# Kernel tuning notes

Hardware: AMD Instinct MI355X
Metric: run time of the kernel (lower is better)

## Reference

```python
import jax, jax.numpy as jnp
import numpy as np

B, S, H = 1, 2048, 2048
HD, NQ, NKV = 128, 16, 4
FFH = 8192
EPS = 1e-5
ROPE_BASE = 10000.0
SOFTMAX_CAP = 50.0
CLIP_L, CLIP_R = 0.0, 1.0


def setup_inputs() -> dict:
    key = jax.random.key(0)
    ks = jax.random.split(key, 10)
    std = 0.02
    return {
        "x": jax.random.normal(ks[0], (B, S, H), dtype=jnp.float32),
        "attn_norm_w": jax.random.uniform(ks[1], (H,), minval=-1.0, maxval=1.0, dtype=jnp.float32),
        "mlp_norm_w": jax.random.uniform(ks[2], (H,), minval=-1.0, maxval=1.0, dtype=jnp.float32),
        "wq": jax.random.normal(ks[3], (H, NQ * HD), dtype=jnp.float32) * std,
        "wk": jax.random.normal(ks[4], (H, NKV * HD), dtype=jnp.float32) * std,
        "wv": jax.random.normal(ks[5], (H, NKV * HD), dtype=jnp.float32) * std,
        "wo": jax.random.normal(ks[6], (NQ * HD, H), dtype=jnp.float32) * std,
        "w_gate": jax.random.normal(ks[7], (H, FFH), dtype=jnp.float32) * std,
        "w_up": jax.random.normal(ks[8], (H, FFH), dtype=jnp.float32) * std,
        "w_down": jax.random.normal(ks[9], (FFH, H), dtype=jnp.float32) * std,
    }


def _rms_norm(x, w):
    # GroupRMSNorm with group_size=None -> whole hidden dim
    var = jnp.mean(jnp.square(x), axis=-1, keepdims=True)
    return x * jax.lax.rsqrt(var + EPS) * w


def _rope_cos_sin(seq_len, dim):
    inv_freq = 1.0 / (ROPE_BASE ** (jnp.arange(0, dim, 2, dtype=jnp.float32) / dim))
    t = jnp.arange(seq_len, dtype=jnp.float32)
    freqs = jnp.outer(t, inv_freq)                      # [S, dim/2]
    emb = jnp.concatenate([freqs, freqs], axis=-1)      # [S, dim]
    return jnp.cos(emb), jnp.sin(emb)


def _apply_rope(x, cos, sin):
    # x: [B, S, h, d]; rotate-half (LLaMA-style)
    d = x.shape[-1]
    x1, x2 = x[..., : d // 2], x[..., d // 2 :]
    rot = jnp.concatenate([-x2, x1], axis=-1)
    return x * cos[None, :, None, :] + rot * sin[None, :, None, :]


def _qk_norm(x):
    # per-head RMS norm over head_dim (qk_norm_group_size == head_dim), unit weight
    var = jnp.mean(jnp.square(x), axis=-1, keepdims=True)
    return x * jax.lax.rsqrt(var + EPS)


def reference(x, attn_norm_w, mlp_norm_w, wq, wk, wv, wo, w_gate, w_up, w_down):
    # ---- attention sub-layer ----
    h = _rms_norm(x, attn_norm_w)                                     # [B,S,H]
    q = (h @ wq).reshape(B, S, NQ, HD)
    k = (h @ wk).reshape(B, S, NKV, HD)
    v = (h @ wv).reshape(B, S, NKV, HD)

    cos, sin = _rope_cos_sin(S, HD)
    q = _apply_rope(q, cos, sin)
    k = _apply_rope(k, cos, sin)

    q = _qk_norm(q)
    k = _qk_norm(k)

    # GQA: expand kv heads to match q heads
    rep = NQ // NKV
    k = jnp.repeat(k, rep, axis=2)                                    # [B,S,NQ,HD]
    v = jnp.repeat(v, rep, axis=2)

    scale = 1.0 / jnp.sqrt(jnp.float32(HD))
    scores = jnp.einsum("bshd,bthd->bhst", q, k) * scale              # [B,NQ,S,S]
    # softmax cap: cap * tanh(s / cap)
    scores = SOFTMAX_CAP * jnp.tanh(scores / SOFTMAX_CAP)
    causal = jnp.tril(jnp.ones((S, S), dtype=bool))
    scores = jnp.where(causal[None, None], scores, -jnp.inf)
    p = jax.nn.softmax(scores, axis=-1)
    # clip range (l, r): clamp(p * (r - l) + l, 0, 1)
    p = jnp.clip(p * (CLIP_R - CLIP_L) + CLIP_L, 0.0, 1.0)
    o = jnp.einsum("bhst,bthd->bshd", p, v).reshape(B, S, NQ * HD)
    x = x + o @ wo

    # ---- MLP sub-layer (gated SiLU) ----
    h2 = _rms_norm(x, mlp_norm_w)
    mlp_out = (jax.nn.silu(h2 @ w_gate) * (h2 @ w_up)) @ w_down
    return x + mlp_out
```

## Files before the change

### kernel.cpp

```cpp
#include <hip/hip_runtime.h>

typedef __bf16 bf16;
typedef __bf16 bf16x4 __attribute__((ext_vector_type(4)));
typedef __bf16 bf16x8 __attribute__((ext_vector_type(8)));
typedef float f32x4 __attribute__((ext_vector_type(4)));

#define GLP16(gp, lp) __builtin_amdgcn_global_load_lds( \
    (const __attribute__((address_space(1))) void*)(gp), \
    (__attribute__((address_space(3))) void*)(lp), 16, 0, 0)

__device__ __forceinline__ f32x4 mfma16(bf16x8 a, bf16x8 b, f32x4 c) {
    return __builtin_amdgcn_mfma_f32_16x16x32_bf16(a, b, c, 0, 0, 0);
}

__global__ __launch_bounds__(256) void k_rmsnorm(const float* __restrict__ x,
        const float* __restrict__ w, bf16* __restrict__ out) {
    const int H = 2048;
    size_t row = blockIdx.x;
    const float* xr = x + row * H;
    int base = threadIdx.x * 8;
    float4 a = *(const float4*)(xr + base);
    float4 b = *(const float4*)(xr + base + 4);
    float ss = a.x*a.x + a.y*a.y + a.z*a.z + a.w*a.w
             + b.x*b.x + b.y*b.y + b.z*b.z + b.w*b.w;
#pragma unroll
    for (int m = 32; m > 0; m >>= 1) ss += __shfl_xor(ss, m);
    __shared__ float red[4];
    if ((threadIdx.x & 63) == 0) red[threadIdx.x >> 6] = ss;
    __syncthreads();
    float tot = red[0] + red[1] + red[2] + red[3];
    float rs = rsqrtf(tot * (1.0f / H) + 1e-5f);
    float4 wa = *(const float4*)(w + base);
    float4 wb = *(const float4*)(w + base + 4);
    bf16x8 ov;
    ov[0] = (bf16)(a.x * rs * wa.x); ov[1] = (bf16)(a.y * rs * wa.y);
    ov[2] = (bf16)(a.z * rs * wa.z); ov[3] = (bf16)(a.w * rs * wa.w);
    ov[4] = (bf16)(b.x * rs * wb.x); ov[5] = (bf16)(b.y * rs * wb.y);
    ov[6] = (bf16)(b.z * rs * wb.z); ov[7] = (bf16)(b.w * rs * wb.w);
    *(bf16x8*)(out + row * H + base) = ov;
}

__global__ __launch_bounds__(256) void k_convT(const float* __restrict__ W,
        bf16* __restrict__ Wt, int K, int N, int rmul, int roff) {
    __shared__ float t[64][65];
    int k0 = blockIdx.x * 64, n0 = blockIdx.y * 64;
    int tid = threadIdx.x;
#pragma unroll
    for (int it = 0; it < 4; it++) {
        int idx = it * 256 + tid;
        int r = idx >> 4, c = (idx & 15) * 4;
        float4 v = *(const float4*)(W + (size_t)(k0 + r) * N + n0 + c);
        t[r][c] = v.x; t[r][c + 1] = v.y; t[r][c + 2] = v.z; t[r][c + 3] = v.w;
    }
    __syncthreads();
#pragma unroll
    for (int it = 0; it < 4; it++) {
        int idx = it * 256 + tid;
        int n = idx >> 4, kc = (idx & 15) * 4;
        bf16x4 o;
#pragma unroll
        for (int j = 0; j < 4; j++) o[j] = (bf16)t[kc + j][n];
        *(bf16x4*)(Wt + ((size_t)(n0 + n) * rmul + roff) * K + k0 + kc) = o;
    }
}

__global__ __launch_bounds__(256) void k_transpose(const bf16* __restrict__ in,
        bf16* __restrict__ out, int R, int C) {
    __shared__ bf16 t[32][33];
    int r0 = blockIdx.x * 32, c0 = blockIdx.y * 32;
    int tx = threadIdx.x & 31, ty = threadIdx.x >> 5;
#pragma unroll
    for (int i = 0; i < 4; i++)
        t[ty + i * 8][tx] = in[(size_t)(r0 + ty + i * 8) * C + c0 + tx];
    __syncthreads();
#pragma unroll
    for (int i = 0; i < 4; i++)
        out[(size_t)(c0 + ty + i * 8) * R + r0 + tx] = t[tx][ty + i * 8];
}

template<int EPI>
__global__ __launch_bounds__(512, 2) void k_gemm5(const bf16* __restrict__ A,
        const bf16* __restrict__ Bt, void* __restrict__ outp,
        const void* __restrict__ aux, int M, int N, int K, int ksplit) {
    extern __shared__ char lds[];
    const int tid = threadIdx.x, wave = tid >> 6, lane = tid & 63;
    const int lr = lane & 15, kg = lane >> 4;
    const int wm = wave >> 2, wn = wave & 3;
    const int bn = blockIdx.x, bm = blockIdx.y, split = blockIdx.z;
    const int row0 = bm * 256, col0 = bn * 256;
    const int kbeg = split * ksplit;
    const int NT = ksplit >> 6;
    const size_t K2 = (size_t)K * 2;
    const int xorm = (lr & 7) << 4;

    char* const A0p = lds;
    char* const A1p = lds + 32768;
    char* const B0p = lds + 65536;
    char* const B1p = lds + 98304;

    size_t soff[2];
#pragma unroll
    for (int s = 0; s < 2; s++) {
        int d = s * 8192 + tid * 16;
        int rh = d >> 7, c = d & 127;
        soff[s] = (size_t)rh * K2 + (c ^ ((rh & 7) << 4));
    }
    const char* Ab = (const char*)A + ((size_t)row0 * K + kbeg) * 2;
    const char* Bb = (const char*)Bt + ((size_t)col0 * K + kbeg) * 2;

    auto stA = [&](int t, int mh) {
        const char* src = Ab + (size_t)(mh * 128) * K2 + (size_t)t * 128;
        char* dst = lds + (t & 1) * 32768 + mh * 16384 + wave * 1024;
        GLP16(src + soff[0], dst);
        GLP16(src + soff[1], dst + 8192);
    };
    auto stB = [&](int t, int nh) {
        const char* src = Bb + (size_t)(nh * 128) * K2 + (size_t)t * 128;
        char* dst = lds + 65536 + (t & 1) * 32768 + nh * 16384 + wave * 1024;
        GLP16(src + soff[0], dst);
        GLP16(src + soff[1], dst + 8192);
    };

    f32x4 acc[8][4];
#pragma unroll
    for (int m = 0; m < 8; m++)
#pragma unroll
        for (int n = 0; n < 4; n++) acc[m][n] = (f32x4){0, 0, 0, 0};

    bf16x8 a[8], c0[4], c1[4];
    auto rdA = [&](const char* base, int mh) {
#pragma unroll
        for (int mi = 0; mi < 4; mi++)
#pragma unroll
            for (int kk = 0; kk < 2; kk++) {
                int rh = wm * 64 + mi * 16 + lr;
                int c = (kk * 64 + kg * 16) ^ xorm;
                a[mi * 2 + kk] = *(const bf16x8*)(base + mh * 16384 + rh * 128 + c);
            }
    };
    auto rdB = [&](const char* base, int nh, bf16x8 (&b)[4]) {
#pragma unroll
        for (int nj = 0; nj < 2; nj++)
#pragma unroll
            for (int kk = 0; kk < 2; kk++) {
                int rh = wn * 32 + nj * 16 + lr;
                int c = (kk * 64 + kg * 16) ^ xorm;
                b[nj * 2 + kk] = *(const bf16x8*)(base + nh * 16384 + rh * 128 + c);
            }
    };
    auto mm = [&](int mh, int nh, bf16x8 (&b)[4]) {
#pragma unroll
        for (int mi = 0; mi < 4; mi++)
#pragma unroll
            for (int nj = 0; nj < 2; nj++)
#pragma unroll
                for (int kk = 0; kk < 2; kk++)
                    acc[mh * 4 + mi][nh * 2 + nj] =
                        mfma16(a[mi * 2 + kk], b[nj * 2 + kk],
                               acc[mh * 4 + mi][nh * 2 + nj]);
    };

#define PBAR do { asm volatile("" ::: "memory"); \
                  __builtin_amdgcn_s_barrier(); \
                  asm volatile("" ::: "memory"); } while (0)

    stA(0, 0); stB(0, 0); stB(0, 1); stA(0, 1);
    stA(1, 0); stB(1, 0); stB(1, 1);
    asm volatile("s_waitcnt vmcnt(6)" ::: "memory");
    PBAR;

    const int NIT = NT >> 1;
    for (int it = 0; it < NIT; ++it) {
        const int t = it * 2;
        const bool more = (t + 2 < NT);
        rdA(A0p, 0); rdB(B0p, 0, c0);
        stA(t + 1, 1);
        __builtin_amdgcn_s_setprio(1); mm(0, 0, c0); __builtin_amdgcn_s_setprio(0);
        PBAR;
        rdB(B0p, 1, c1);
        if (more) stA(t + 2, 0);
        __builtin_amdgcn_s_setprio(1); mm(0, 1, c1); __builtin_amdgcn_s_setprio(0);
        PBAR;
        rdA(A0p, 1);
        if (more) stB(t + 2, 0);
        __builtin_amdgcn_s_setprio(1); mm(1, 1, c1); __builtin_amdgcn_s_setprio(0);
        PBAR;
        if (more) stB(t + 2, 1);
        __builtin_amdgcn_s_setprio(1); mm(1, 0, c0); __builtin_amdgcn_s_setprio(0);
        if (more) asm volatile("s_waitcnt vmcnt(6)" ::: "memory");
        else      asm volatile("s_waitcnt vmcnt(0)" ::: "memory");
        PBAR;
        rdA(A1p, 0); rdB(B1p, 0, c0);
        if (more) stA(t + 2, 1);
        __builtin_amdgcn_s_setprio(1); mm(0, 0, c0); __builtin_amdgcn_s_setprio(0);
        PBAR;
        rdB(B1p, 1, c1);
        if (t + 3 < NT) stA(t + 3, 0);
        __builtin_amdgcn_s_setprio(1); mm(0, 1, c1); __builtin_amdgcn_s_setprio(0);
        PBAR;
        rdA(A1p, 1);
        if (t + 3 < NT) stB(t + 3, 0);
        __builtin_amdgcn_s_setprio(1); mm(1, 1, c1); __builtin_amdgcn_s_setprio(0);
        PBAR;
        if (t + 3 < NT) stB(t + 3, 1);
        __builtin_amdgcn_s_setprio(1); mm(1, 0, c0); __builtin_amdgcn_s_setprio(0);
        if (more) asm volatile("s_waitcnt vmcnt(6)" ::: "memory");
        PBAR;
    }
#undef PBAR

#pragma unroll
    for (int mi = 0; mi < 8; mi++)
#pragma unroll
        for (int ni = 0; ni < 4; ni++)
#pragma unroll
            for (int r = 0; r < 4; r++) {
                size_t row = row0 + (mi >> 2) * 128 + wm * 64 + (mi & 3) * 16 + kg * 4 + r;
                size_t col = col0 + (ni >> 1) * 128 + wn * 32 + (ni & 1) * 16 + lr;
                float vv = acc[mi][ni][r];
                if (EPI == 5) {
                    ((bf16*)outp)[(size_t)split * M * N + row * N + col] = (bf16)vv;
                } else {
                    float pv = __shfl_xor(vv, 1);
                    float g = (lane & 1) ? pv : vv;
                    float u = (lane & 1) ? vv : pv;
                    float sg = g / (1.0f + __expf(-g));
                    if (!(lane & 1))
                        ((bf16*)outp)[row * (size_t)(N >> 1) + (col >> 1)] =
                            (bf16)(sg * u);
                }
            }
}

__global__ __launch_bounds__(256) void k_reduce(const bf16* __restrict__ parts,
        const float* __restrict__ resid, float* __restrict__ out,
        int ns, size_t n8) {
    size_t i = (size_t)blockIdx.x * 256 + threadIdx.x;
    if (i >= n8) return;
    size_t base = i * 8;
    float4 a = *(const float4*)(resid + base);
    float4 b = *(const float4*)(resid + base + 4);
    for (int s = 0; s < ns; s++) {
        bf16x8 p = *(const bf16x8*)(parts + (size_t)s * n8 * 8 + base);
        a.x += (float)p[0]; a.y += (float)p[1]; a.z += (float)p[2]; a.w += (float)p[3];
        b.x += (float)p[4]; b.y += (float)p[5]; b.z += (float)p[6]; b.w += (float)p[7];
    }
    *(float4*)(out + base) = a;
    *(float4*)(out + base + 4) = b;
}

__global__ __launch_bounds__(256) void k_reduce_rms(const bf16* __restrict__ parts,
        const float* __restrict__ resid, const float* __restrict__ w,
        float* __restrict__ x2, bf16* __restrict__ hb, int ns) {
    const int H = 2048;
    size_t row = blockIdx.x;
    int base = threadIdx.x * 8;
    const float* rr = resid + row * H + base;
    float4 a = *(const float4*)rr;
    float4 b = *(const float4*)(rr + 4);
    for (int s = 0; s < ns; s++) {
        bf16x8 p = *(const bf16x8*)(parts + (size_t)s * H * 2048 + row * H + base);
        a.x += (float)p[0]; a.y += (float)p[1]; a.z += (float)p[2]; a.w += (float)p[3];
        b.x += (float)p[4]; b.y += (float)p[5]; b.z += (float)p[6]; b.w += (float)p[7];
    }
    *(float4*)(x2 + row * H + base) = a;
    *(float4*)(x2 + row * H + base + 4) = b;
    float ss = a.x*a.x + a.y*a.y + a.z*a.z + a.w*a.w
             + b.x*b.x + b.y*b.y + b.z*b.z + b.w*b.w;
#pragma unroll
    for (int m = 32; m > 0; m >>= 1) ss += __shfl_xor(ss, m);
    __shared__ float red[4];
    if ((threadIdx.x & 63) == 0) red[threadIdx.x >> 6] = ss;
    __syncthreads();
    float tot = red[0] + red[1] + red[2] + red[3];
    float rs = rsqrtf(tot * (1.0f / H) + 1e-5f);
    float4 wa = *(const float4*)(w + base);
    float4 wb = *(const float4*)(w + base + 4);
    bf16x8 ov;
    ov[0] = (bf16)(a.x * rs * wa.x); ov[1] = (bf16)(a.y * rs * wa.y);
    ov[2] = (bf16)(a.z * rs * wa.z); ov[3] = (bf16)(a.w * rs * wa.w);
    ov[4] = (bf16)(b.x * rs * wb.x); ov[5] = (bf16)(b.y * rs * wb.y);
    ov[6] = (bf16)(b.z * rs * wb.z); ov[7] = (bf16)(b.w * rs * wb.w);
    *(bf16x8*)(hb + row * H + base) = ov;
}

__global__ __launch_bounds__(256) void k_qkvrope(const bf16* __restrict__ parts,
        bf16* __restrict__ qb, bf16* __restrict__ kb, bf16* __restrict__ vb) {
    int s = blockIdx.x;
    int tid = threadIdx.x, wave = tid >> 6, lane = tid & 63;
    const bf16* p0 = parts + (size_t)s * 3072;
    const bf16* p1 = p0 + (size_t)2048 * 3072;
    float f = exp2f((float)lane * -0.2076205059304601f);
    float sn, cs;
    sincosf((float)s * f, &sn, &cs);
#pragma unroll 1
    for (int pass = 0; pass < 5; pass++) {
        int h = pass * 4 + wave;
        int base = (h < 16) ? h * 128 : 2048 + (h - 16) * 128;
        int c1 = base + lane, c2 = c1 + 64;
        float x1 = (float)p0[c1] + (float)p1[c1];
        float x2 = (float)p0[c2] + (float)p1[c2];
        float o1 = x1 * cs - x2 * sn;
        float o2 = x2 * cs + x1 * sn;
        float ss = o1 * o1 + o2 * o2;
#pragma unroll
        for (int m = 32; m > 0; m >>= 1) ss += __shfl_xor(ss, m);
        float rs = rsqrtf(ss * (1.0f / 128.0f) + 1e-5f);
        bf16* dst = (h < 16) ? (qb + (size_t)s * 2048 + h * 128)
                             : (kb + (size_t)s * 512 + (h - 16) * 128);
        dst[lane] = (bf16)(o1 * rs);
        dst[lane + 64] = (bf16)(o2 * rs);
    }
    int c = 2560 + tid * 2;
    float v0 = (float)p0[c] + (float)p1[c];
    float v1 = (float)p0[c + 1] + (float)p1[c + 1];
    bf16* vd = vb + (size_t)s * 512 + tid * 2;
    vd[0] = (bf16)v0; vd[1] = (bf16)v1;
}

__global__ __launch_bounds__(256, 2) void k_attn(const bf16* __restrict__ qg,
        const bf16* __restrict__ kgl, const bf16* __restrict__ vtg,
        bf16* __restrict__ og) {
    extern __shared__ char alds[];
    int pi = blockIdx.x, h = blockIdx.y, kvh = h >> 2;
    int qt = (pi & 1) ? (31 - (pi >> 1)) : (pi >> 1);
    int nt = qt + 1;
    int tid = threadIdx.x, wave = tid >> 6, lane = tid & 63;
    int lr = lane & 15, kgrp = lane >> 4;

    int rowQ[4], colQ[4], rowV[4], colV[4];
#pragma unroll
    for (int j = 0; j < 4; j++) {
        int p = j * 4096 + wave * 1024 + lane * 16;
        int ps = p ^ (((p >> 8) & 7) << 4);
        rowQ[j] = ps >> 8; colQ[j] = ps & 255;
        int pv = p ^ (((p >> 7) & 7) << 4);
        rowV[j] = pv >> 7; colV[j] = pv & 127;
    }

    const float C1 = 0.08838834764831845f / 50.0f;
    const float L2E50 = 72.13475204444817f;

#pragma unroll
    for (int j = 0; j < 4; j++)
        GLP16((const char*)qg + (size_t)(qt * 64 + rowQ[j]) * 4096 + h * 256 + colQ[j],
              alds + j * 4096 + wave * 1024);
    for (int t = 0; t < 2 && t < nt; t++) {
#pragma unroll
        for (int j = 0; j < 4; j++)
            GLP16((const char*)kgl + (size_t)(t * 64 + rowQ[j]) * 1024 + kvh * 256 + colQ[j],
                  alds + 16384 + t * 16384 + j * 4096 + wave * 1024);
#pragma unroll
        for (int j = 0; j < 4; j++)
            GLP16((const char*)vtg + (size_t)(kvh * 128 + rowV[j]) * 4096 + t * 128 + colV[j],
                  alds + 49152 + t * 16384 + j * 4096 + wave * 1024);
    }
    if (nt > 1) asm volatile("s_waitcnt vmcnt(8)" ::: "memory");
    else        asm volatile("s_waitcnt vmcnt(0)" ::: "memory");
    __builtin_amdgcn_s_barrier();

    bf16x8 qf[4];
#pragma unroll
    for (int c = 0; c < 4; c++) {
        int b = (wave * 16 + lr) * 256 + c * 64 + kgrp * 16;
        qf[c] = *(const bf16x8*)(alds + (b ^ (((b >> 8) & 7) << 4)));
    }
    __builtin_amdgcn_s_barrier();

    f32x4 accO[8];
#pragma unroll
    for (int n = 0; n < 8; n++) accO[n] = (f32x4){0, 0, 0, 0};
    float lsum[4] = {0, 0, 0, 0};
    int qrow = qt * 64 + wave * 16 + kgrp * 4;

    for (int kt = 0; kt < nt; kt++) {
        int buf = kt & 1;
        const char* Kb = alds + 16384 + buf * 16384;
        const char* Vb = alds + 49152 + buf * 16384;
        char* Pb = alds;
#pragma unroll
        for (int j = 0; j < 4; j++) {
            f32x4 s = {0, 0, 0, 0};
#pragma unroll
            for (int c = 0; c < 4; c++) {
                int b = (j * 16 + lr) * 256 + c * 64 + kgrp * 16;
                bf16x8 kf = *(const bf16x8*)(Kb + (b ^ (((b >> 8) & 7) << 4)));
                s = mfma16(qf[c], kf, s);
            }
            int key = kt * 64 + j * 16 + lr;
#pragma unroll
            for (int r = 0; r < 4; r++) {
                float y = s[r] * C1;
                float y2 = y * y;
                float u = fmaf(y2, 0.13333333f, -0.33333333f);
                u = fmaf(y2, u, 1.0f);
                float t5 = y * u;
                float pe = fmaf(t5, L2E50, -L2E50);
                float pv = (key <= qrow + r) ? exp2f(pe) : 0.0f;
                lsum[r] += pv;
                int wb = (wave * 16 + kgrp * 4 + r) * 128 + (j * 16 + lr) * 2;
                *(bf16*)(Pb + (wb ^ (((wb >> 7) & 7) << 4))) = (bf16)pv;
            }
        }
        bf16x8 pf[2];
#pragma unroll
        for (int ks2 = 0; ks2 < 2; ks2++) {
            int b = (wave * 16 + lr) * 128 + ks2 * 64 + kgrp * 16;
            pf[ks2] = *(const bf16x8*)(Pb + (b ^ (((b >> 7) & 7) << 4)));
        }
#pragma unroll
        for (int n = 0; n < 8; n++)
#pragma unroll
            for (int ks2 = 0; ks2 < 2; ks2++) {
                int b = (n * 16 + lr) * 128 + ks2 * 64 + kgrp * 16;
                bf16x8 vf = *(const bf16x8*)(Vb + (b ^ (((b >> 7) & 7) << 4)));
                accO[n] = mfma16(pf[ks2], vf, accO[n]);
            }
        __builtin_amdgcn_s_barrier();
        bool more = (kt + 2 < nt);
        if (more) {
            int t = kt + 2;
#pragma unroll
            for (int j = 0; j < 4; j++)
                GLP16((const char*)kgl + (size_t)(t * 64 + rowQ[j]) * 1024 + kvh * 256 + colQ[j],
                      alds + 16384 + buf * 16384 + j * 4096 + wave * 1024);
#pragma unroll
            for (int j = 0; j < 4; j++)
                GLP16((const char*)vtg + (size_t)(kvh * 128 + rowV[j]) * 4096 + t * 128 + colV[j],
                      alds + 49152 + buf * 16384 + j * 4096 + wave * 1024);
        }
        if (kt + 1 < nt) {
            if (more) asm volatile("s_waitcnt vmcnt(8)" ::: "memory");
            else      asm volatile("s_waitcnt vmcnt(0)" ::: "memory");
            __builtin_amdgcn_s_barrier();
        }
    }
#pragma unroll
    for (int r = 0; r < 4; r++) {
        float t = lsum[r];
        t += __shfl_xor(t, 1); t += __shfl_xor(t, 2);
        t += __shfl_xor(t, 4); t += __shfl_xor(t, 8);
        lsum[r] = t;
    }
#pragma unroll
    for (int n = 0; n < 8; n++)
#pragma unroll
        for (int r = 0; r < 4; r++) {
            size_t row = qt * 64 + wave * 16 + kgrp * 4 + r;
            og[row * 2048 + h * 128 + n * 16 + lr] = (bf16)(accO[n][r] / lsum[r]);
        }
}

extern "C" void kernel_launch(void* const* d_in, const int* in_sizes, int n_in,
                              void* d_out, int out_size, void* d_ws, size_t ws_size,
                              hipStream_t stream) {
    const float* x      = (const float*)d_in[0];
    const float* attn_w = (const float*)d_in[1];
    const float* mlp_w  = (const float*)d_in[2];
    const float* wq     = (const float*)d_in[3];
    const float* wk     = (const float*)d_in[4];
    const float* wv     = (const float*)d_in[5];
    const float* wo     = (const float*)d_in[6];
    const float* wgate  = (const float*)d_in[7];
    const float* wup    = (const float*)d_in[8];
    const float* wdown  = (const float*)d_in[9];
    float* out = (float*)d_out;
    char* ws = (char*)d_ws;

    const size_t MB = 1024 * 1024;
    bf16* Wqkv = (bf16*)(ws + 0);
    bf16* vt   = (bf16*)(ws + 0);
    bf16* pO   = (bf16*)(ws + 0);
    bf16* Wgu  = (bf16*)(ws + 0);
    bf16* pD   = (bf16*)(ws + 0);
    bf16* WoT  = (bf16*)(ws + 64 * MB);
    bf16* WdT  = (bf16*)(ws + 64 * MB);
    bf16* hb   = (bf16*)(ws + 96 * MB);
    bf16* qb   = (bf16*)(ws + 104 * MB);
    bf16* kb   = (bf16*)(ws + 112 * MB);
    bf16* vb   = (bf16*)(ws + 114 * MB);
    bf16* ob   = (bf16*)(ws + 116 * MB);
    float* x2  = (float*)(ws + 124 * MB);
    bf16* gb   = (bf16*)(ws + 140 * MB);
    bf16* pQ   = (bf16*)(ws + 172 * MB);

    const int LDS5 = 131072;
    hipFuncSetAttribute((const void*)&k_gemm5<4>,
        hipFuncAttributeMaxDynamicSharedMemorySize, LDS5);
    hipFuncSetAttribute((const void*)&k_gemm5<5>,
        hipFuncAttributeMaxDynamicSharedMemorySize, LDS5);
    const int LDSA = 81920;
    hipFuncSetAttribute((const void*)&k_attn,
        hipFuncAttributeMaxDynamicSharedMemorySize, LDSA);

    const size_t n8 = (size_t)2048 * 2048 / 8;

    k_rmsnorm<<<2048, 256, 0, stream>>>(x, attn_w, hb);
    k_convT<<<dim3(32, 32), 256, 0, stream>>>(wq, Wqkv, 2048, 2048, 1, 0);
    k_convT<<<dim3(32, 8), 256, 0, stream>>>(wk, Wqkv + 4194304, 2048, 512, 1, 0);
    k_convT<<<dim3(32, 8), 256, 0, stream>>>(wv, Wqkv + 5242880, 2048, 512, 1, 0);
    k_gemm5<5><<<dim3(12, 8, 2), 512, LDS5, stream>>>(hb, Wqkv, pQ, nullptr,
                                                      2048, 3072, 2048, 1024);
    k_qkvrope<<<2048, 256, 0, stream>>>(pQ, qb, kb, vb);
    k_transpose<<<dim3(64, 16), 256, 0, stream>>>(vb, vt, 2048, 512);
    k_attn<<<dim3(32, 16), 256, LDSA, stream>>>(qb, kb, vt, ob);
    k_convT<<<dim3(32, 32), 256, 0, stream>>>(wo, WoT, 2048, 2048, 1, 0);
    k_gemm5<5><<<dim3(8, 8, 4), 512, LDS5, stream>>>(ob, WoT, pO, nullptr,
                                                     2048, 2048, 2048, 512);
    k_reduce_rms<<<2048, 256, 0, stream>>>(pO, x, mlp_w, x2, hb, 4);
    k_convT<<<dim3(32, 128), 256, 0, stream>>>(wgate, Wgu, 2048, 8192, 2, 0);
    k_convT<<<dim3(32, 128), 256, 0, stream>>>(wup, Wgu, 2048, 8192, 2, 1);
    k_gemm5<4><<<dim3(64, 8, 1), 512, LDS5, stream>>>(hb, Wgu, gb, nullptr,
                                                      2048, 16384, 2048, 2048);
    k_convT<<<dim3(128, 32), 256, 0, stream>>>(wdown, WdT, 8192, 2048, 1, 0);
    k_gemm5<5><<<dim3(8, 8, 4), 512, LDS5, stream>>>(gb, WdT, pD, nullptr,
                                                     2048, 2048, 8192, 2048);
    k_reduce<<<2048, 256, 0, stream>>>(pD, x2, out, 4, n8);
}
```

Baseline: 441.6 us.

## Simplify GEMM main loop to plain double-buffered pipeline with two barriers per tile

Replaces the staggered eight-phase GEMM loop, which interleaved partial tile loads with the MFMA quarters, with a simpler loop. Each iteration reads the current buffer, issues all loads for the next tile up front, runs two halves of the MFMA work, then waits for all loads with vmcnt(0). This cuts barriers from four to two per tile and simplifies scheduling. In exchange it gives up the finer-grained overlap and prefetch depth, and the full vmcnt(0) wait can expose memory latency.

```diff
diff --git a/kernel.cpp b/kernel.cpp
--- a/kernel.cpp
+++ b/kernel.cpp
@@ -79,7 +79,7 @@
 }
 
 template<int EPI>
-__global__ __launch_bounds__(512, 2) void k_gemm5(const bf16* __restrict__ A,
+__global__ __launch_bounds__(512, 2) void k_gemm8(const bf16* __restrict__ A,
         const bf16* __restrict__ Bt, void* __restrict__ outp,
         const void* __restrict__ aux, int M, int N, int K, int ksplit) {
     extern __shared__ char lds[];
@@ -93,11 +93,6 @@
     const size_t K2 = (size_t)K * 2;
     const int xorm = (lr & 7) << 4;
 
-    char* const A0p = lds;
-    char* const A1p = lds + 32768;
-    char* const B0p = lds + 65536;
-    char* const B1p = lds + 98304;
-
     size_t soff[2];
 #pragma unroll
     for (int s = 0; s < 2; s++) {
@@ -164,47 +159,25 @@
                   __builtin_amdgcn_s_barrier(); \
                   asm volatile("" ::: "memory"); } while (0)
 
-    stA(0, 0); stB(0, 0); stB(0, 1); stA(0, 1);
-    stA(1, 0); stB(1, 0); stB(1, 1);
-    asm volatile("s_waitcnt vmcnt(6)" ::: "memory");
+    stA(0, 0); stA(0, 1); stB(0, 0); stB(0, 1);
+    asm volatile("s_waitcnt vmcnt(0)" ::: "memory");
     PBAR;
 
-    const int NIT = NT >> 1;
-    for (int it = 0; it < NIT; ++it) {
-        const int t = it * 2;
-        const bool more = (t + 2 < NT);
-        rdA(A0p, 0); rdB(B0p, 0, c0);
-        stA(t + 1, 1);
-        __builtin_amdgcn_s_setprio(1); mm(0, 0, c0); __builtin_amdgcn_s_setprio(0);
+    for (int t = 0; t < NT; ++t) {
+        const char* Ac = lds + (t & 1) * 32768;
+        const char* Bc = lds + 65536 + (t & 1) * 32768;
+        const bool m1 = (t + 1 < NT);
+        rdA(Ac, 0); rdB(Bc, 0, c0); rdB(Bc, 1, c1);
+        if (m1) { stA(t + 1, 0); stA(t + 1, 1); stB(t + 1, 0); stB(t + 1, 1); }
+        __builtin_amdgcn_s_setprio(1);
+        mm(0, 0, c0); mm(0, 1, c1);
+        __builtin_amdgcn_s_setprio(0);
         PBAR;
-        rdB(B0p, 1, c1);
-        if (more) stA(t + 2, 0);
-        __builtin_amdgcn_s_setprio(1); mm(0, 1, c1); __builtin_amdgcn_s_setprio(0);
-        PBAR;
-        rdA(A0p, 1);
-        if (more) stB(t + 2, 0);
-        __builtin_amdgcn_s_setprio(1); mm(1, 1, c1); __builtin_amdgcn_s_setprio(0);
-        PBAR;
-        if (more) stB(t + 2, 1);
-        __builtin_amdgcn_s_setprio(1); mm(1, 0, c0); __builtin_amdgcn_s_setprio(0);
-        if (more) asm volatile("s_waitcnt vmcnt(6)" ::: "memory");
-        else      asm volatile("s_waitcnt vmcnt(0)" ::: "memory");
-        PBAR;
-        rdA(A1p, 0); rdB(B1p, 0, c0);
-        if (more) stA(t + 2, 1);
-        __builtin_amdgcn_s_setprio(1); mm(0, 0, c0); __builtin_amdgcn_s_setprio(0);
-        PBAR;
-        rdB(B1p, 1, c1);
-        if (t + 3 < NT) stA(t + 3, 0);
-        __builtin_amdgcn_s_setprio(1); mm(0, 1, c1); __builtin_amdgcn_s_setprio(0);
-        PBAR;
-        rdA(A1p, 1);
-        if (t + 3 < NT) stB(t + 3, 0);
-        __builtin_amdgcn_s_setprio(1); mm(1, 1, c1); __builtin_amdgcn_s_setprio(0);
-        PBAR;
-        if (t + 3 < NT) stB(t + 3, 1);
-        __builtin_amdgcn_s_setprio(1); mm(1, 0, c0); __builtin_amdgcn_s_setprio(0);
-        if (more) asm volatile("s_waitcnt vmcnt(6)" ::: "memory");
+        rdA(Ac, 1);
+        __builtin_amdgcn_s_setprio(1);
+        mm(1, 0, c0); mm(1, 1, c1);
+        __builtin_amdgcn_s_setprio(0);
+        if (m1) asm volatile("s_waitcnt vmcnt(0)" ::: "memory");
         PBAR;
     }
 #undef PBAR
@@ -484,11 +457,11 @@
     bf16* gb   = (bf16*)(ws + 140 * MB);
     bf16* pQ   = (bf16*)(ws + 172 * MB);
 
-    const int LDS5 = 131072;
-    hipFuncSetAttribute((const void*)&k_gemm5<4>,
-        hipFuncAttributeMaxDynamicSharedMemorySize, LDS5);
-    hipFuncSetAttribute((const void*)&k_gemm5<5>,
-        hipFuncAttributeMaxDynamicSharedMemorySize, LDS5);
+    const int LDS8 = 131072;
+    hipFuncSetAttribute((const void*)&k_gemm8<4>,
+        hipFuncAttributeMaxDynamicSharedMemorySize, LDS8);
+    hipFuncSetAttribute((const void*)&k_gemm8<5>,
+        hipFuncAttributeMaxDynamicSharedMemorySize, LDS8);
     const int LDSA = 81920;
     hipFuncSetAttribute((const void*)&k_attn,
         hipFuncAttributeMaxDynamicSharedMemorySize, LDSA);
@@ -499,21 +472,21 @@
     k_convT<<<dim3(32, 32), 256, 0, stream>>>(wq, Wqkv, 2048, 2048, 1, 0);
     k_convT<<<dim3(32, 8), 256, 0, stream>>>(wk, Wqkv + 4194304, 2048, 512, 1, 0);
     k_convT<<<dim3(32, 8), 256, 0, stream>>>(wv, Wqkv + 5242880, 2048, 512, 1, 0);
-    k_gemm5<5><<<dim3(12, 8, 2), 512, LDS5, stream>>>(hb, Wqkv, pQ, nullptr,
+    k_gemm8<5><<<dim3(12, 8, 2), 512, LDS8, stream>>>(hb, Wqkv, pQ, nullptr,
                                                       2048, 3072, 2048, 1024);
     k_qkvrope<<<2048, 256, 0, stream>>>(pQ, qb, kb, vb);
     k_transpose<<<dim3(64, 16), 256, 0, stream>>>(vb, vt, 2048, 512);
     k_attn<<<dim3(32, 16), 256, LDSA, stream>>>(qb, kb, vt, ob);
     k_convT<<<dim3(32, 32), 256, 0, stream>>>(wo, WoT, 2048, 2048, 1, 0);
-    k_gemm5<5><<<dim3(8, 8, 4), 512, LDS5, stream>>>(ob, WoT, pO, nullptr,
+    k_gemm8<5><<<dim3(8, 8, 4), 512, LDS8, stream>>>(ob, WoT, pO, nullptr,
                                                      2048, 2048, 2048, 512);
     k_reduce_rms<<<2048, 256, 0, stream>>>(pO, x, mlp_w, x2, hb, 4);
     k_convT<<<dim3(32, 128), 256, 0, stream>>>(wgate, Wgu, 2048, 8192, 2, 0);
     k_convT<<<dim3(32, 128), 256, 0, stream>>>(wup, Wgu, 2048, 8192, 2, 1);
-    k_gemm5<4><<<dim3(64, 8, 1), 512, LDS5, stream>>>(hb, Wgu, gb, nullptr,
+    k_gemm8<4><<<dim3(64, 8, 1), 512, LDS8, stream>>>(hb, Wgu, gb, nullptr,
                                                       2048, 16384, 2048, 2048);
     k_convT<<<dim3(128, 32), 256, 0, stream>>>(wdown, WdT, 8192, 2048, 1, 0);
-    k_gemm5<5><<<dim3(8, 8, 4), 512, LDS5, stream>>>(gb, WdT, pD, nullptr,
+    k_gemm8<5><<<dim3(8, 8, 4), 512, LDS8, stream>>>(gb, WdT, pD, nullptr,
                                                      2048, 2048, 8192, 2048);
     k_reduce<<<2048, 256, 0, stream>>>(pD, x2, out, 4, n8);
 }
```

Measured after the change: 438.2 us (median of 3 runs). No clear change (-0.8%).
